# Kernel optimization log

Measured on AMD Instinct MI355X. Metric: run time of the kernel, lower is better.

## Reference

```python
import jax, jax.numpy as jnp
import numpy as np

MAX_ITER = 10   # float32 branch of cg()
TOL = 1e-10

def _cdot(a, b):
    # complex_dot: sum(conj(a) * b) over all elements
    return jnp.sum(jnp.conj(a) * b)

def _A(p, smaps, mask):
    # p: [H,W] complex, smaps: [C,H,W] complex, mask: [H,W] real
    return jnp.fft.fft2(smaps * p[None], norm='ortho') * mask[None]

def _AH(y, smaps, mask):
    imgs = jnp.fft.ifft2(y * mask[None], norm='ortho')
    return jnp.sum(jnp.conj(smaps) * imgs, axis=0)  # [H,W]

def _cg(M, rhs):
    # conjugate gradient, faithful to the TF while_loop body
    def cond(s):
        i, rTr, x, r, p = s
        return jnp.logical_and(i < MAX_ITER, rTr > TOL)
    def body(s):
        i, rTr, x, r, p = s
        Ap = M(p)
        alpha = rTr / jnp.real(_cdot(p, Ap))
        x = x + p * alpha
        r = r - Ap * alpha
        rTrNew = jnp.real(_cdot(r, r))
        beta = rTrNew / rTr
        p = r + p * beta
        return (i + 1, rTrNew, x, r, p)
    rTr0 = jnp.real(_cdot(rhs, rhs))
    s0 = (jnp.int32(0), rTr0, jnp.zeros_like(rhs), rhs, rhs)
    return jax.lax.while_loop(cond, body, s0)[2]

def _solve_one(lambdaa, rhs, smaps, mask):
    M = lambda p: _AH(_A(p, smaps, mask), smaps, mask) + p * lambdaa
    return _cg(M, rhs)

_solve_b = jax.vmap(_solve_one, in_axes=(None, 0, 0, 0))  # replaces map_fn
_AH_b = jax.vmap(_AH, in_axes=(0, 0, 0))

def setup_inputs():
    key = jax.random.key(0)
    ks = jax.random.split(key, 7)
    B, C, H, W = 4, 16, 384, 384
    f = lambda k, s: jax.random.normal(k, s, dtype=jnp.float32)
    return {
        'lambdaa': 0.05 * jnp.ones((), jnp.float32),
        'x_re': f(ks[0], (B, H, W)),
        'x_im': f(ks[1], (B, H, W)),
        'y_re': f(ks[2], (B, C, H, W)),
        'y_im': f(ks[3], (B, C, H, W)),
        'smaps_re': f(ks[4], (B, C, H, W)),
        'smaps_im': f(ks[5], (B, C, H, W)),
        'mask': (jax.random.uniform(ks[6], (B, H, W)) < 0.33).astype(jnp.float32),
    }

def reference(lambdaa, x_re, x_im, y_re, y_im, smaps_re, smaps_im, mask):
    x = jax.lax.complex(x_re, x_im)
    y = jax.lax.complex(y_re, y_im)
    smaps = jax.lax.complex(smaps_re, smaps_im)
    # rhs = AH(y) + lambdaa * x
    rhs = _AH_b(y, smaps, mask) + x * lambdaa
    out = _solve_b(lambdaa, rhs, smaps, mask)  # [B,H,W] complex
    return jnp.stack([out.real, out.imag], axis=-1)  # [B,H,W,2] float32
```

## Files before the change

kernel.cpp:

```cpp
#include <hip/hip_runtime.h>
#include <hip/hip_fp16.h>


#define Bn 4
#define Cn 16
#define Hn 384
#define Wn 384
#define NPIX (Hn*Wn)
#define NPIX2 (NPIX/2)
#define TPB 256
#define CTPB 512
#define NCOL 16
#define TOLF 1e-10f
#define NITER 10
#define RED_BLKS 72
#define GRP 4
#define CPG 4
#define RPITCH 416
#define CPITCH 417

__device__ __forceinline__ float2 cadd(float2 a, float2 b){ return make_float2(a.x+b.x, a.y+b.y); }
__device__ __forceinline__ float2 csub(float2 a, float2 b){ return make_float2(a.x-b.x, a.y-b.y); }
__device__ __forceinline__ float2 cmulf(float2 a, float2 b){
  return make_float2(a.x*b.x - a.y*b.y, a.x*b.y + a.y*b.x);
}

__device__ __forceinline__ void wave_fence(){ asm volatile("s_waitcnt lgkmcnt(0)" ::: "memory"); }

template<int IMM>
__device__ __forceinline__ float2 shx(float2 v){
  int x = __builtin_amdgcn_ds_swizzle(__float_as_int(v.x), IMM);
  int y = __builtin_amdgcn_ds_swizzle(__float_as_int(v.y), IMM);
  return make_float2(__int_as_float(x), __int_as_float(y));
}

template<int CTRL>
__device__ __forceinline__ float2 dpp2(float2 v){
  int x = __builtin_amdgcn_mov_dpp(__float_as_int(v.x), CTRL, 0xF, 0xF, true);
  int y = __builtin_amdgcn_mov_dpp(__float_as_int(v.y), CTRL, 0xF, 0xF, true);
  return make_float2(__int_as_float(x), __int_as_float(y));
}
__device__ __forceinline__ float2 xchg1 (float2 v){ return dpp2<0xB1>(v);  }
__device__ __forceinline__ float2 xchg2 (float2 v){ return dpp2<0x4E>(v);  }
__device__ __forceinline__ float2 xchg4 (float2 v){ return dpp2<0x1B>(dpp2<0x141>(v)); }
__device__ __forceinline__ float2 xchg8 (float2 v){ return dpp2<0x128>(v); }
__device__ __forceinline__ float2 xchg16(float2 v){ return shx<0x401F>(v); }

__device__ __forceinline__ int rev5(int x){
  return ((x&1)<<4) | ((x&2)<<2) | (x&4) | ((x&8)>>2) | ((x&16)>>4);
}

__device__ __forceinline__ int offmap(int w){ return w + ((w*683)>>13); }

template<int DIR>
__device__ __forceinline__ void fft12(float2* v)
{
  const float S3 = (DIR<0) ? -0.86602540378443864676f : 0.86602540378443864676f;
  const float sg = (DIR<0) ? -1.f : 1.f;
  float2 t[4][3];
#pragma unroll
  for (int b = 0; b < 4; ++b) {
    float2 a0 = v[b], a1 = v[4+b], a2 = v[8+b];
    float2 s = cadd(a1,a2), d = csub(a1,a2);
    float2 mm = make_float2(a0.x - 0.5f*s.x, a0.y - 0.5f*s.y);
    float2 e  = make_float2(-d.y*S3, d.x*S3);
    t[b][0] = cadd(a0,s);
    t[b][1] = cadd(mm,e);
    t[b][2] = csub(mm,e);
  }
  const float2 w1  = make_float2(0.86602540378443864676f, sg*0.5f);
  const float2 w2  = make_float2(0.5f, sg*0.86602540378443864676f);
  const float2 w3  = make_float2(0.f, sg);
  const float2 w4t = make_float2(-0.5f, sg*0.86602540378443864676f);
  const float2 w6  = make_float2(-1.f, 0.f);
  t[1][1] = cmulf(t[1][1], w1);  t[1][2] = cmulf(t[1][2], w2);
  t[2][1] = cmulf(t[2][1], w2);  t[2][2] = cmulf(t[2][2], w4t);
  t[3][1] = cmulf(t[3][1], w3);  t[3][2] = cmulf(t[3][2], w6);
#pragma unroll
  for (int c = 0; c < 3; ++c) {
    float2 e = cadd(t[0][c], t[2][c]);
    float2 f = csub(t[0][c], t[2][c]);
    float2 g = cadd(t[1][c], t[3][c]);
    float2 h = csub(t[1][c], t[3][c]);
    float2 ih = (DIR<0) ? make_float2(h.y, -h.x) : make_float2(-h.y, h.x);
    v[c]   = cadd(e,g);
    v[c+3] = cadd(f,ih);
    v[c+6] = csub(e,g);
    v[c+9] = csub(f,ih);
  }
}

template<int DIR>
__device__ __forceinline__ void fft32_lanes(float2* v, int li)
{
  const float c2pi = (DIR<0) ? -6.2831853071795864769f : 6.2831853071795864769f;
  const float sg   = (DIR<0) ? -1.f : 1.f;
  float s, c;
  __sincosf(c2pi*(1.f/32.f)*(float)(li&15), &s, &c); float2 wA = make_float2(c,s);
  __sincosf(c2pi*(1.f/16.f)*(float)(li&7),  &s, &c); float2 wB = make_float2(c,s);
  __sincosf(c2pi*(1.f/ 8.f)*(float)(li&3),  &s, &c); float2 wC = make_float2(c,s);
  bool bA = li & 16, bB = li & 8, bC = li & 4, bD = li & 2, bE = li & 1;
#pragma unroll
  for (int k = 0; k < 12; ++k) {
    float2 a = v[k], o;
    o = xchg16(a); a = bA ? cmulf(csub(o,a), wA) : cadd(a,o);
    o = xchg8 (a); a = bB ? cmulf(csub(o,a), wB) : cadd(a,o);
    o = xchg4 (a); a = bC ? cmulf(csub(o,a), wC) : cadd(a,o);
    o = xchg2 (a);
    { float2 su = cadd(a,o), d = csub(o,a);
      float2 dw = bE ? make_float2(-sg*d.y, sg*d.x) : d;
      a = bD ? dw : su; }
    o = xchg1 (a); a = bE ? csub(o,a) : cadd(a,o);
    v[k] = a;
  }
}

template<int DIR>
__device__ __forceinline__ void fft32_lanes_dit(float2* v, int li)
{
  const float c2pi = (DIR<0) ? -6.2831853071795864769f : 6.2831853071795864769f;
  const float sg   = (DIR<0) ? -1.f : 1.f;
  float s, c;
  __sincosf(c2pi*(1.f/32.f)*(float)(li&15), &s, &c); float2 wA = make_float2(c,s);
  __sincosf(c2pi*(1.f/16.f)*(float)(li&7),  &s, &c); float2 wB = make_float2(c,s);
  __sincosf(c2pi*(1.f/ 8.f)*(float)(li&3),  &s, &c); float2 wC = make_float2(c,s);
  bool bA = li & 16, bB = li & 8, bC = li & 4, bD = li & 2, bE = li & 1;
#pragma unroll
  for (int k = 0; k < 12; ++k) {
    float2 a = v[k], o;
    o = xchg1(a); a = bE ? csub(o,a) : cadd(a,o);
    { float2 aw = make_float2(-sg*a.y, sg*a.x);
      a = (bD && bE) ? aw : a;
      o = xchg2(a); a = bD ? csub(o,a) : cadd(a,o); }
    { float2 aw = cmulf(a, wC); a = bC ? aw : a;
      o = xchg4(a); a = bC ? csub(o,a) : cadd(a,o); }
    { float2 aw = cmulf(a, wB); a = bB ? aw : a;
      o = xchg8(a); a = bB ? csub(o,a) : cadd(a,o); }
    { float2 aw = cmulf(a, wA); a = bA ? aw : a;
      o = xchg16(a); a = bA ? csub(o,a) : cadd(a,o); }
    v[k] = a;
  }
}

template<int DIR>
__device__ __forceinline__ void fft384(float2* v, int li)
{
  fft12<DIR>(v);
  const float c2pi = (DIR<0) ? -6.2831853071795864769f : 6.2831853071795864769f;
  float s, c;
  __sincosf(c2pi*(1.f/384.f)*(float)li, &s, &c);
  float2 W = make_float2(c,s), cw = W;
#pragma unroll
  for (int k = 1; k < 12; ++k) { v[k] = cmulf(v[k], cw); cw = cmulf(cw, W); }
  fft32_lanes<DIR>(v, li);
}

template<int DIR>
__device__ __forceinline__ void fft384_scr(float2* v, int li)
{
  fft32_lanes_dit<DIR>(v, li);
  const float c2pi = (DIR<0) ? -6.2831853071795864769f : 6.2831853071795864769f;
  float s, c;
  __sincosf(c2pi*(1.f/384.f)*(float)li, &s, &c);
  float2 W = make_float2(c,s), cw = W;
#pragma unroll
  for (int k = 1; k < 12; ++k) { v[k] = cmulf(v[k], cw); cw = cmulf(cw, W); }
  fft12<DIR>(v);
}


template<bool HS>
__global__ __launch_bounds__(TPB) void k_row_fwd(
    const float2* __restrict__ p, const float* __restrict__ Sre,
    const float* __restrict__ Sim, const __half2* __restrict__ Sh,
    __half2* __restrict__ tmp)
{
  int tid = threadIdx.x;
  int wave = tid>>6, lane = tid&63, sub = lane>>5, li = lane&31;
  int row = wave*2 + sub;
  int tile = blockIdx.x % (Hn/8);
  int bc   = blockIdx.x / (Hn/8);
  int b = bc / Cn;
  int h = tile*8 + row;
  size_t gbase = (size_t)bc*NPIX + (size_t)h*Wn;
  size_t pbase = (size_t)b*NPIX + (size_t)h*Wn;

  float2 v[12];
#pragma unroll
  for (int k = 0; k < 12; ++k) {
    int w = 32*k + li;
    float2 pv = p[pbase + w];
    float sr, si;
    if (HS) { float2 sv = __half22float2(Sh[gbase + w]); sr = sv.x; si = sv.y; }
    else    { sr = Sre[gbase + w]; si = Sim[gbase + w]; }
    v[k] = make_float2(sr*pv.x - si*pv.y, sr*pv.y + si*pv.x);
  }
  fft384<-1>(v, li);
#pragma unroll
  for (int k = 0; k < 12; ++k)
    tmp[gbase + 32*k + li] = __float22half2_rn(v[k]);
}

template<bool HS>
__global__ __launch_bounds__(TPB) void k_row_inv_scr(
    const __half2* __restrict__ tmp, const float* __restrict__ Sre,
    const float* __restrict__ Sim, const __half2* __restrict__ Sh,
    float2* __restrict__ partial)
{
  int tid = threadIdx.x;
  int wave = tid>>6, lane = tid&63, sub = lane>>5, li = lane&31;
  int row = wave*2 + sub;
  int tile = blockIdx.x % (Hn/8);
  int rest = blockIdx.x / (Hn/8);
  int g = rest % GRP;
  int b = rest / GRP;
  int h = tile*8 + row;

  size_t gbase0 = ((size_t)b*Cn + g*CPG)*NPIX + (size_t)h*Wn;
  __half2 hb[12];
#pragma unroll
  for (int k = 0; k < 12; ++k) hb[k] = tmp[gbase0 + 32*k + li];

  float2 acc[12];
#pragma unroll
  for (int k = 0; k < 12; ++k) acc[k] = make_float2(0.f, 0.f);

  for (int j = 0; j < CPG; ++j) {
    size_t gb = gbase0 + (size_t)j*NPIX;
    float2 vc[12];
#pragma unroll
    for (int k = 0; k < 12; ++k) vc[k] = __half22float2(hb[k]);
    if (j + 1 < CPG) {
      size_t gbn = gb + NPIX;
#pragma unroll
      for (int k = 0; k < 12; ++k) hb[k] = tmp[gbn + 32*k + li];
    }
    fft384_scr<1>(vc, li);
#pragma unroll
    for (int k = 0; k < 12; ++k) {
      int w = 32*k + li;
      float sr, si;
      if (HS) { float2 sv = __half22float2(Sh[gb + w]); sr = sv.x; si = sv.y; }
      else    { sr = Sre[gb + w]; si = Sim[gb + w]; }
      acc[k].x += sr*vc[k].x + si*vc[k].y;
      acc[k].y += sr*vc[k].y - si*vc[k].x;
    }
  }
  size_t pbase = ((size_t)g*Bn + b)*NPIX + (size_t)h*Wn;
#pragma unroll
  for (int k = 0; k < 12; ++k) partial[pbase + 32*k + li] = acc[k];
}

__global__ __launch_bounds__(TPB) void k_row_inv_nat(
    const __half2* __restrict__ tmp, const float* __restrict__ Sre,
    const float* __restrict__ Sim, float2* __restrict__ partial)
{
  __shared__ float2 lbuf[8*RPITCH];
  int tid = threadIdx.x;
  int wave = tid>>6, lane = tid&63, sub = lane>>5, li = lane&31;
  int row = wave*2 + sub;
  int tile = blockIdx.x % (Hn/8);
  int rest = blockIdx.x / (Hn/8);
  int g = rest % GRP;
  int b = rest / GRP;
  int h = tile*8 + row;
  int m = rev5(li);
  float2* lrow = lbuf + row*RPITCH;

  size_t gbase0 = ((size_t)b*Cn + g*CPG)*NPIX + (size_t)h*Wn;
  __half2 hb[12];
#pragma unroll
  for (int k = 0; k < 12; ++k) hb[k] = tmp[gbase0 + 32*k + li];

  float2 acc[12];
#pragma unroll
  for (int k = 0; k < 12; ++k) acc[k] = make_float2(0.f, 0.f);

  for (int j = 0; j < CPG; ++j) {
    size_t gb = gbase0 + (size_t)j*NPIX;
    float2 vc[12];
#pragma unroll
    for (int k = 0; k < 12; ++k) vc[k] = __half22float2(hb[k]);
    if (j + 1 < CPG) {
      size_t gbn = gb + NPIX;
#pragma unroll
      for (int k = 0; k < 12; ++k) hb[k] = tmp[gbn + 32*k + li];
    }
    fft384<1>(vc, li);
    wave_fence();
#pragma unroll
    for (int k = 0; k < 12; ++k) lrow[13*m + k] = vc[k];
    wave_fence();
#pragma unroll
    for (int k = 0; k < 12; ++k) {
      int w = 32*k + li;
      float2 u = lrow[offmap(w)];
      float sr = Sre[gb + w], si = Sim[gb + w];
      acc[k].x += sr*u.x + si*u.y;
      acc[k].y += sr*u.y - si*u.x;
    }
  }
  size_t pbase = ((size_t)g*Bn + b)*NPIX + (size_t)h*Wn;
#pragma unroll
  for (int k = 0; k < 12; ++k) partial[pbase + 32*k + li] = acc[k];
}

__global__ __launch_bounds__(TPB) void k_spack(
    const float* __restrict__ sre, const float* __restrict__ sim,
    __half2* __restrict__ sh)
{
  size_t i = (size_t)blockIdx.x*TPB + threadIdx.x;
  if (i < (size_t)Bn*Cn*NPIX) sh[i] = __floats2half2_rn(sre[i], sim[i]);
}

__global__ __launch_bounds__(TPB) void k_maskp(
    const float* __restrict__ mask, float* __restrict__ maskP,
    float* __restrict__ scal)
{
  int idx = blockIdx.x*TPB + threadIdx.x;
  if (blockIdx.x == 0) scal[threadIdx.x] = 0.0f;
  if (idx >= Bn*NPIX) return;
  int k = idx % 12; int t = idx / 12;
  int li = t & 31; t >>= 5;
  int wa = t % Wn; int b = t / Wn;
  int wt = (wa >> 5) + 12*rev5(wa & 31);
  maskP[idx] = mask[((size_t)b*Hn + (k + 12*rev5(li)))*Wn + wt] * (1.0f/(float)NPIX);
}

__global__ __launch_bounds__(CTPB) void k_col_full(
    __half2* __restrict__ tmp, const float* __restrict__ maskP)
{
  __shared__ __half2 dbuf[NCOL*CPITCH];
  int tid = threadIdx.x;
  int wave = tid>>6, lane = tid&63, sub = lane>>5, li = lane&31;
  int col = wave*2 + sub;
  int tile = blockIdx.x % (Wn/NCOL);
  int bc   = blockIdx.x / (Wn/NCOL);
  int b = bc / Cn;
  int w0 = tile*NCOL;
  size_t tbase = (size_t)bc*NPIX;

  for (int e = tid; e < NCOL*Hn; e += CTPB) {
    int wi = e & (NCOL-1), h = e >> 4;
    dbuf[wi*CPITCH + offmap(h)] = tmp[tbase + (size_t)h*Wn + w0 + wi];
  }
  __syncthreads();

  __half2* drow = dbuf + col*CPITCH;
  int w = w0 + col;
  const float4* mp4 = (const float4*)(maskP + (((size_t)b*Wn + w)*32 + li)*12);
  float4 m0 = mp4[0], m1 = mp4[1], m2 = mp4[2];
  float2 v[12];
#pragma unroll
  for (int k = 0; k < 12; ++k) v[k] = __half22float2(drow[offmap(32*k + li)]);
  fft384<-1>(v, li);
  float mk[12] = {m0.x,m0.y,m0.z,m0.w, m1.x,m1.y,m1.z,m1.w, m2.x,m2.y,m2.z,m2.w};
#pragma unroll
  for (int k = 0; k < 12; ++k) v[k] = make_float2(v[k].x*mk[k], v[k].y*mk[k]);
  fft384_scr<1>(v, li);
#pragma unroll
  for (int k = 0; k < 12; ++k) drow[offmap(32*k + li)] = __float22half2_rn(v[k]);
  __syncthreads();

  for (int e = tid; e < NCOL*Hn; e += CTPB) {
    int wi = e & (NCOL-1), h = e >> 4;
    tmp[tbase + (size_t)h*Wn + w0 + wi] = dbuf[wi*CPITCH + offmap(h)];
  }
}

__global__ __launch_bounds__(CTPB) void k_col_rhs(
    const float* __restrict__ yre, const float* __restrict__ yim,
    const float* __restrict__ mask, __half2* __restrict__ tmp)
{
  __shared__ float2 dbuf[NCOL*CPITCH];
  int tid = threadIdx.x;
  int wave = tid>>6, lane = tid&63, sub = lane>>5, li = lane&31;
  int col = wave*2 + sub;
  int tile = blockIdx.x % (Wn/NCOL);
  int bc   = blockIdx.x / (Wn/NCOL);
  int b = bc / Cn;
  int w0 = tile*NCOL;
  size_t tbase = (size_t)bc*NPIX;
  size_t mbase = (size_t)b*NPIX;

  for (int e = tid; e < NCOL*Hn; e += CTPB) {
    int wi = e & (NCOL-1), h = e >> 4;
    size_t gi = (size_t)h*Wn + w0 + wi;
    float mv = mask[mbase + gi] * (1.0f/384.0f);
    dbuf[wi*CPITCH + offmap(h)] = make_float2(yre[tbase+gi]*mv, yim[tbase+gi]*mv);
  }
  __syncthreads();

  float2* drow = dbuf + col*CPITCH;
  int m = rev5(li);
  float2 v[12];
#pragma unroll
  for (int k = 0; k < 12; ++k) v[k] = drow[offmap(32*k + li)];
  fft384<1>(v, li);
  wave_fence();
#pragma unroll
  for (int k = 0; k < 12; ++k) drow[13*m + k] = v[k];
  __syncthreads();

  for (int e = tid; e < NCOL*Hn; e += CTPB) {
    int wi = e & (NCOL-1), h = e >> 4;
    tmp[tbase + (size_t)h*Wn + w0 + wi] = __float22half2_rn(dbuf[wi*CPITCH + offmap(h)]);
  }
}


__device__ __forceinline__ void block_reduce_atomic(float sum, float* target)
{
  __shared__ float red[TPB];
  red[threadIdx.x] = sum; __syncthreads();
  for (int s = TPB/2; s > 0; s >>= 1) {
    if (threadIdx.x < s) red[threadIdx.x] += red[threadIdx.x + s];
    __syncthreads();
  }
  if (threadIdx.x == 0) unsafeAtomicAdd(target, red[0]);
  __syncthreads();
}

__global__ __launch_bounds__(TPB) void k_rhs_init(
    const float* __restrict__ xre, const float* __restrict__ xim,
    const float* __restrict__ lam, const float2* __restrict__ partial,
    float2* __restrict__ r, float2* __restrict__ p, float2* __restrict__ x,
    float* __restrict__ scal)
{
  int b = blockIdx.y;
  float l = lam[0];
  float sum = 0.0f;
  const float2* xr2 = (const float2*)(xre + (size_t)b*NPIX);
  const float2* xi2 = (const float2*)(xim + (size_t)b*NPIX);
  float4* r4 = (float4*)(r + (size_t)b*NPIX);
  float4* p4 = (float4*)(p + (size_t)b*NPIX);
  float4* x4 = (float4*)(x + (size_t)b*NPIX);
  for (int i = blockIdx.x*TPB + threadIdx.x; i < NPIX2; i += RED_BLKS*TPB) {
    float2 re = xr2[i], im = xi2[i];
    float4 rv = make_float4(l*re.x, l*im.x, l*re.y, l*im.y);
#pragma unroll
    for (int g = 0; g < GRP; ++g) {
      float4 pv = ((const float4*)(partial + ((size_t)g*Bn + b)*NPIX))[i];
      rv.x += pv.x; rv.y += pv.y; rv.z += pv.z; rv.w += pv.w;
    }
    r4[i] = rv; p4[i] = rv;
    x4[i] = make_float4(0.f, 0.f, 0.f, 0.f);
    sum += rv.x*rv.x + rv.y*rv.y + rv.z*rv.z + rv.w*rv.w;
  }
  block_reduce_atomic(sum, &scal[b]);
}

__global__ __launch_bounds__(TPB) void k_combine_dot3(
    const float2* __restrict__ p, const float2* __restrict__ r,
    const float* __restrict__ lam, const float2* __restrict__ partial,
    float2* __restrict__ Ap, float* __restrict__ slot)
{
  int b = blockIdx.y;
  float l = lam[0];
  float s_pAp = 0.f, s_AA = 0.f, s_rA = 0.f;
  const float4* p4 = (const float4*)(p + (size_t)b*NPIX);
  const float4* r4 = (const float4*)(r + (size_t)b*NPIX);
  float4* A4 = (float4*)(Ap + (size_t)b*NPIX);
  for (int i = blockIdx.x*TPB + threadIdx.x; i < NPIX2; i += RED_BLKS*TPB) {
    float4 pv = p4[i];
    float4 av = make_float4(l*pv.x, l*pv.y, l*pv.z, l*pv.w);
#pragma unroll
    for (int g = 0; g < GRP; ++g) {
      float4 qv = ((const float4*)(partial + ((size_t)g*Bn + b)*NPIX))[i];
      av.x += qv.x; av.y += qv.y; av.z += qv.z; av.w += qv.w;
    }
    A4[i] = av;
    float4 rv = r4[i];
    s_pAp += pv.x*av.x + pv.y*av.y + pv.z*av.z + pv.w*av.w;
    s_AA  += av.x*av.x + av.y*av.y + av.z*av.z + av.w*av.w;
    s_rA  += rv.x*av.x + rv.y*av.y + rv.z*av.z + rv.w*av.w;
  }
  block_reduce_atomic(s_pAp, &slot[b]);
  block_reduce_atomic(s_AA,  &slot[4+b]);
  block_reduce_atomic(s_rA,  &slot[8+b]);
}

__global__ __launch_bounds__(TPB) void k_upd(
    float2* __restrict__ x, float2* __restrict__ r, float2* __restrict__ p,
    const float2* __restrict__ Ap, float* __restrict__ scal, int it)
{
  int b = blockIdx.y;
  float rtr = scal[it*4 + b];
  const float* slot = scal + 64 + it*12;
  bool act = rtr > TOLF;
  float alpha = act ? rtr / slot[b] : 0.f;
  float rtrn = act ? fmaxf(rtr - 2.f*alpha*slot[8+b] + alpha*alpha*slot[4+b], 0.f) : rtr;
  float beta = act ? rtrn / rtr : 0.f;
  if (blockIdx.x == 0 && threadIdx.x == 0) scal[(it+1)*4 + b] = rtrn;
  if (!act) return;
  float4* x4 = (float4*)(x + (size_t)b*NPIX);
  float4* r4 = (float4*)(r + (size_t)b*NPIX);
  float4* p4 = (float4*)(p + (size_t)b*NPIX);
  const float4* A4 = (const float4*)(Ap + (size_t)b*NPIX);
  for (int i = blockIdx.x*TPB + threadIdx.x; i < NPIX2; i += RED_BLKS*TPB) {
    float4 pv = p4[i], av = A4[i], xv = x4[i], rv = r4[i];
    xv.x += alpha*pv.x; xv.y += alpha*pv.y; xv.z += alpha*pv.z; xv.w += alpha*pv.w;
    rv.x -= alpha*av.x; rv.y -= alpha*av.y; rv.z -= alpha*av.z; rv.w -= alpha*av.w;
    x4[i] = xv; r4[i] = rv;
    p4[i] = make_float4(rv.x + beta*pv.x, rv.y + beta*pv.y,
                        rv.z + beta*pv.z, rv.w + beta*pv.w);
  }
}


extern "C" void kernel_launch(void* const* d_in, const int* in_sizes, int n_in,
                              void* d_out, int out_size, void* d_ws, size_t ws_size,
                              hipStream_t stream)
{
  const float* lam  = (const float*)d_in[0];
  const float* xre  = (const float*)d_in[1];
  const float* xim  = (const float*)d_in[2];
  const float* yre  = (const float*)d_in[3];
  const float* yim  = (const float*)d_in[4];
  const float* sre  = (const float*)d_in[5];
  const float* sim  = (const float*)d_in[6];
  const float* mask = (const float*)d_in[7];

  const size_t szTmp  = (size_t)Bn*Cn*NPIX*sizeof(__half2);
  const size_t szVec  = (size_t)Bn*NPIX*sizeof(float2);
  const size_t szMask = (size_t)Bn*NPIX*sizeof(float);
  const size_t szSh   = (size_t)Bn*Cn*NPIX*sizeof(__half2);
  const size_t base   = szTmp + (size_t)GRP*szVec + 3*szVec + 2048 + szMask;
  const bool useSh    = (ws_size >= base + szSh);

  char* ws = (char*)d_ws;
  __half2* tmp = (__half2*)ws;  ws += szTmp;
  float2* part = (float2*)ws;   ws += (size_t)GRP*szVec;
  float2* r    = (float2*)ws;   ws += szVec;
  float2* p    = (float2*)ws;   ws += szVec;
  float2* Ap   = (float2*)ws;   ws += szVec;
  float*  scal = (float*)ws;    ws += 2048;
  float*  mskP = (float*)ws;    ws += szMask;
  __half2* Sh  = (__half2*)ws;
  float2* x    = (float2*)d_out;

  dim3 blk(TPB);
  dim3 rg(RED_BLKS, Bn);
  int grid_row = Bn*Cn*(Hn/8);
  int grid_col = Bn*Cn*(Wn/NCOL);
  int grid_inv = Bn*GRP*(Hn/8);

  k_maskp<<<(Bn*NPIX)/TPB, blk, 0, stream>>>(mask, mskP, scal);
  if (useSh)
    k_spack<<<(Bn*Cn*NPIX)/TPB, blk, 0, stream>>>(sre, sim, Sh);

  k_col_rhs<<<grid_col, CTPB, 0, stream>>>(yre, yim, mask, tmp);
  k_row_inv_nat<<<grid_inv, blk, 0, stream>>>(tmp, sre, sim, part);
  k_rhs_init<<<rg, blk, 0, stream>>>(xre, xim, lam, part, r, p, x, scal);

  for (int it = 0; it < NITER; ++it) {
    if (useSh) {
      k_row_fwd<true><<<grid_row, blk, 0, stream>>>(p, sre, sim, Sh, tmp);
      k_col_full<<<grid_col, CTPB, 0, stream>>>(tmp, mskP);
      k_row_inv_scr<true><<<grid_inv, blk, 0, stream>>>(tmp, sre, sim, Sh, part);
    } else {
      k_row_fwd<false><<<grid_row, blk, 0, stream>>>(p, sre, sim, Sh, tmp);
      k_col_full<<<grid_col, CTPB, 0, stream>>>(tmp, mskP);
      k_row_inv_scr<false><<<grid_inv, blk, 0, stream>>>(tmp, sre, sim, Sh, part);
    }
    k_combine_dot3<<<rg, blk, 0, stream>>>(p, r, lam, part, Ap, scal + 64 + it*12);
    k_upd<<<rg, blk, 0, stream>>>(x, r, p, Ap, scal, it);
  }
}
```

Measured before the change: 1.393 ms.

## Process two columns per thread pair in column FFT kernel with 256-thread blocks

The column FFT kernel now runs 256 threads per block, with each 32-lane group transforming two columns interleaved so the mask loads and FFT work of one overlap the other. Launch bounds request 6 blocks per CU, and the LDS pitch changes to 415 for the half2 buffer. The twiddle multiplication also changes from a serial chain to a tree of powers, which shortens the dependency chain. The added instruction-level parallelism comes at the cost of doubled register arrays, which may push register pressure against the occupancy hint.

```diff
diff --git a/kernel.cpp b/kernel.cpp
--- a/kernel.cpp
+++ b/kernel.cpp
@@ -9,7 +9,8 @@
 #define NPIX (Hn*Wn)
 #define NPIX2 (NPIX/2)
 #define TPB 256
-#define CTPB 512
+#define CTPB 256
+#define RTPB 512
 #define NCOL 16
 #define TOLF 1e-10f
 #define NITER 10
@@ -17,7 +18,8 @@
 #define GRP 4
 #define CPG 4
 #define RPITCH 416
-#define CPITCH 417
+#define CPITCH 415
+#define CPITCH_R 417
 
 __device__ __forceinline__ float2 cadd(float2 a, float2 b){ return make_float2(a.x+b.x, a.y+b.y); }
 __device__ __forceinline__ float2 csub(float2 a, float2 b){ return make_float2(a.x-b.x, a.y-b.y); }
@@ -142,6 +144,21 @@
   }
 }
 
+__device__ __forceinline__ void twiddle_chain(float2* v, float2 W1)
+{
+  v[1] = cmulf(v[1], W1);
+  float2 W2 = cmulf(W1,W1); v[2] = cmulf(v[2], W2);
+  float2 W3 = cmulf(W2,W1); v[3] = cmulf(v[3], W3);
+  float2 W4 = cmulf(W2,W2); v[4] = cmulf(v[4], W4);
+  float2 W5 = cmulf(W3,W2); v[5] = cmulf(v[5], W5);
+  float2 W6 = cmulf(W3,W3); v[6] = cmulf(v[6], W6);
+  float2 W7 = cmulf(W4,W3); v[7] = cmulf(v[7], W7);
+  float2 W8 = cmulf(W4,W4); v[8] = cmulf(v[8], W8);
+  v[9]  = cmulf(v[9],  cmulf(W5,W4));
+  v[10] = cmulf(v[10], cmulf(W5,W5));
+  v[11] = cmulf(v[11], cmulf(W6,W5));
+}
+
 template<int DIR>
 __device__ __forceinline__ void fft384(float2* v, int li)
 {
@@ -149,9 +166,7 @@
   const float c2pi = (DIR<0) ? -6.2831853071795864769f : 6.2831853071795864769f;
   float s, c;
   __sincosf(c2pi*(1.f/384.f)*(float)li, &s, &c);
-  float2 W = make_float2(c,s), cw = W;
-#pragma unroll
-  for (int k = 1; k < 12; ++k) { v[k] = cmulf(v[k], cw); cw = cmulf(cw, W); }
+  twiddle_chain(v, make_float2(c,s));
   fft32_lanes<DIR>(v, li);
 }
 
@@ -162,9 +177,7 @@
   const float c2pi = (DIR<0) ? -6.2831853071795864769f : 6.2831853071795864769f;
   float s, c;
   __sincosf(c2pi*(1.f/384.f)*(float)li, &s, &c);
-  float2 W = make_float2(c,s), cw = W;
-#pragma unroll
-  for (int k = 1; k < 12; ++k) { v[k] = cmulf(v[k], cw); cw = cmulf(cw, W); }
+  twiddle_chain(v, make_float2(c,s));
   fft12<DIR>(v);
 }
 
@@ -327,13 +340,13 @@
   maskP[idx] = mask[((size_t)b*Hn + (k + 12*rev5(li)))*Wn + wt] * (1.0f/(float)NPIX);
 }
 
-__global__ __launch_bounds__(CTPB) void k_col_full(
+__global__ __launch_bounds__(CTPB, 6) void k_col_full(
     __half2* __restrict__ tmp, const float* __restrict__ maskP)
 {
   __shared__ __half2 dbuf[NCOL*CPITCH];
   int tid = threadIdx.x;
   int wave = tid>>6, lane = tid&63, sub = lane>>5, li = lane&31;
-  int col = wave*2 + sub;
+  int slot = wave*2 + sub;
   int tile = blockIdx.x % (Wn/NCOL);
   int bc   = blockIdx.x / (Wn/NCOL);
   int b = bc / Cn;
@@ -346,20 +359,40 @@
   }
   __syncthreads();
 
-  __half2* drow = dbuf + col*CPITCH;
-  int w = w0 + col;
-  const float4* mp4 = (const float4*)(maskP + (((size_t)b*Wn + w)*32 + li)*12);
-  float4 m0 = mp4[0], m1 = mp4[1], m2 = mp4[2];
-  float2 v[12];
-#pragma unroll
-  for (int k = 0; k < 12; ++k) v[k] = __half22float2(drow[offmap(32*k + li)]);
-  fft384<-1>(v, li);
-  float mk[12] = {m0.x,m0.y,m0.z,m0.w, m1.x,m1.y,m1.z,m1.w, m2.x,m2.y,m2.z,m2.w};
-#pragma unroll
-  for (int k = 0; k < 12; ++k) v[k] = make_float2(v[k].x*mk[k], v[k].y*mk[k]);
-  fft384_scr<1>(v, li);
-#pragma unroll
-  for (int k = 0; k < 12; ++k) drow[offmap(32*k + li)] = __float22half2_rn(v[k]);
+  __half2* drow0 = dbuf + slot*CPITCH;
+  __half2* drow1 = dbuf + (slot+8)*CPITCH;
+  int wa = w0 + slot, wb = w0 + slot + 8;
+  const float4* mp4a = (const float4*)(maskP + (((size_t)b*Wn + wa)*32 + li)*12);
+  const float4* mp4b = (const float4*)(maskP + (((size_t)b*Wn + wb)*32 + li)*12);
+
+  float2 v0[12], v1[12];
+#pragma unroll
+  for (int k = 0; k < 12; ++k) v0[k] = __half22float2(drow0[offmap(32*k + li)]);
+#pragma unroll
+  for (int k = 0; k < 12; ++k) v1[k] = __half22float2(drow1[offmap(32*k + li)]);
+
+  float4 a0 = mp4a[0], a1 = mp4a[1], a2 = mp4a[2];
+  fft384<-1>(v0, li);
+  float4 b0 = mp4b[0], b1 = mp4b[1], b2 = mp4b[2];
+  fft384<-1>(v1, li);
+
+  {
+    float mk[12] = {a0.x,a0.y,a0.z,a0.w, a1.x,a1.y,a1.z,a1.w, a2.x,a2.y,a2.z,a2.w};
+#pragma unroll
+    for (int k = 0; k < 12; ++k) v0[k] = make_float2(v0[k].x*mk[k], v0[k].y*mk[k]);
+  }
+  fft384_scr<1>(v0, li);
+#pragma unroll
+  for (int k = 0; k < 12; ++k) drow0[offmap(32*k + li)] = __float22half2_rn(v0[k]);
+
+  {
+    float mk[12] = {b0.x,b0.y,b0.z,b0.w, b1.x,b1.y,b1.z,b1.w, b2.x,b2.y,b2.z,b2.w};
+#pragma unroll
+    for (int k = 0; k < 12; ++k) v1[k] = make_float2(v1[k].x*mk[k], v1[k].y*mk[k]);
+  }
+  fft384_scr<1>(v1, li);
+#pragma unroll
+  for (int k = 0; k < 12; ++k) drow1[offmap(32*k + li)] = __float22half2_rn(v1[k]);
   __syncthreads();
 
   for (int e = tid; e < NCOL*Hn; e += CTPB) {
@@ -368,11 +401,11 @@
   }
 }
 
-__global__ __launch_bounds__(CTPB) void k_col_rhs(
+__global__ __launch_bounds__(RTPB) void k_col_rhs(
     const float* __restrict__ yre, const float* __restrict__ yim,
     const float* __restrict__ mask, __half2* __restrict__ tmp)
 {
-  __shared__ float2 dbuf[NCOL*CPITCH];
+  __shared__ float2 dbuf[NCOL*CPITCH_R];
   int tid = threadIdx.x;
   int wave = tid>>6, lane = tid&63, sub = lane>>5, li = lane&31;
   int col = wave*2 + sub;
@@ -383,15 +416,15 @@
   size_t tbase = (size_t)bc*NPIX;
   size_t mbase = (size_t)b*NPIX;
 
-  for (int e = tid; e < NCOL*Hn; e += CTPB) {
+  for (int e = tid; e < NCOL*Hn; e += RTPB) {
     int wi = e & (NCOL-1), h = e >> 4;
     size_t gi = (size_t)h*Wn + w0 + wi;
     float mv = mask[mbase + gi] * (1.0f/384.0f);
-    dbuf[wi*CPITCH + offmap(h)] = make_float2(yre[tbase+gi]*mv, yim[tbase+gi]*mv);
+    dbuf[wi*CPITCH_R + offmap(h)] = make_float2(yre[tbase+gi]*mv, yim[tbase+gi]*mv);
   }
   __syncthreads();
 
-  float2* drow = dbuf + col*CPITCH;
+  float2* drow = dbuf + col*CPITCH_R;
   int m = rev5(li);
   float2 v[12];
 #pragma unroll
@@ -402,9 +435,9 @@
   for (int k = 0; k < 12; ++k) drow[13*m + k] = v[k];
   __syncthreads();
 
-  for (int e = tid; e < NCOL*Hn; e += CTPB) {
+  for (int e = tid; e < NCOL*Hn; e += RTPB) {
     int wi = e & (NCOL-1), h = e >> 4;
-    tmp[tbase + (size_t)h*Wn + w0 + wi] = __float22half2_rn(dbuf[wi*CPITCH + offmap(h)]);
+    tmp[tbase + (size_t)h*Wn + w0 + wi] = __float22half2_rn(dbuf[wi*CPITCH_R + offmap(h)]);
   }
 }
 
@@ -549,7 +582,7 @@
   if (useSh)
     k_spack<<<(Bn*Cn*NPIX)/TPB, blk, 0, stream>>>(sre, sim, Sh);
 
-  k_col_rhs<<<grid_col, CTPB, 0, stream>>>(yre, yim, mask, tmp);
+  k_col_rhs<<<grid_col, RTPB, 0, stream>>>(yre, yim, mask, tmp);
   k_row_inv_nat<<<grid_inv, blk, 0, stream>>>(tmp, sre, sim, part);
   k_rhs_init<<<rg, blk, 0, stream>>>(xre, xim, lam, part, r, p, x, scal);
 
```

Result: slower. 2.402 ms (+72.5%).
